# Kernel tuning notes

Hardware: AMD Instinct MI355X
Metric: run time of the kernel (lower is better)

## Reference

```python
import jax, jax.numpy as jnp
import numpy as np

P = 8  # patch size (hardcoded in unfold/fold of the original module)


def conv2d(x, w, b, groups=1):
    # x: (N,C,H,W), w: (O, C//groups, 3, 3), 'SAME' padding = padding=1 for 3x3
    y = jax.lax.conv_general_dilated(
        x, w, window_strides=(1, 1), padding='SAME',
        dimension_numbers=('NCHW', 'OIHW', 'NCHW'),
        feature_group_count=groups)
    return y + b[None, :, None, None]


def unfold8(x):
    # F.unfold(kernel=8, stride=8): (N,C,H,W) -> (N, C*64, L), channel-major then
    # kernel-row/col ordering, patches in row-major order.
    N, C, H, W = x.shape
    x = x.reshape(N, C, H // P, P, W // P, P)
    x = x.transpose(0, 1, 3, 5, 2, 4)        # N,C,ki,kj,nh,nw
    return x.reshape(N, C * P * P, (H // P) * (W // P))


def fold8(x, H, W):
    # inverse of unfold8 (non-overlapping, stride == kernel)
    N = x.shape[0]
    C = x.shape[1] // (P * P)
    x = x.reshape(N, C, P, P, H // P, W // P)
    x = x.transpose(0, 1, 4, 2, 5, 3)        # N,C,nh,ki,nw,kj
    return x.reshape(N, C, H, W)


def setup_inputs() -> dict:
    key = jax.random.key(0)
    ks = jax.random.split(key, 9)
    c = 64
    x = jax.random.normal(ks[0], (16, 7, c, 64, 64), dtype=jnp.float32)
    wq = jax.random.normal(ks[1], (c, 1, 3, 3), dtype=jnp.float32) * 0.05
    wk = jax.random.normal(ks[2], (c, 1, 3, 3), dtype=jnp.float32) * 0.05
    wv = jax.random.normal(ks[3], (c, c, 3, 3), dtype=jnp.float32) * 0.05
    wc = jax.random.normal(ks[4], (c, c, 3, 3), dtype=jnp.float32) * 0.05
    bq = jnp.zeros((c,), jnp.float32)
    bk = jnp.zeros((c,), jnp.float32)
    bv = jnp.zeros((c,), jnp.float32)
    bc = jnp.zeros((c,), jnp.float32)
    return {"x": x, "wq": wq, "bq": bq, "wk": wk, "bk": bk,
            "wv": wv, "bv": bv, "wc": wc, "bc": bc}


def reference(x, wq, bq, wk, bk, wv, bv, wc, bc):
    heads = 1
    b, t, c, h, w = x.shape
    D = P * P * c          # dim
    d = D // heads         # hidden_dim per head
    L = (h // P) * (w // P)  # num patches per frame

    xf = x.reshape(-1, c, h, w)
    q = unfold8(conv2d(xf, wq, bq, groups=c))   # depthwise conv
    k = unfold8(conv2d(xf, wk, bk, groups=c))   # depthwise conv
    v = unfold8(conv2d(xf, wv, bv))             # dense conv

    def rearr(u):
        # (b*t, D, L) -> (b, heads, d, t*L)
        return u.reshape(b, t, heads, d, L).transpose(0, 2, 3, 1, 4).reshape(b, heads, d, t * L)

    q, k, v = rearr(q), rearr(k), rearr(v)

    attn = jnp.einsum('bhds,bhdu->bhsu', q, k) * (d ** -0.5)  # (b,H,tL,tL)
    attn = jax.nn.softmax(attn, axis=-1)
    out = jnp.einsum('bhsu,bhdu->bhsd', attn, v)               # (b,H,tL,d)

    out = out.reshape(b, heads, t, L, d).transpose(0, 2, 1, 4, 3).reshape(b * t, D, L)
    feat = fold8(out, h, w)
    return conv2d(feat, wc, bc).reshape(x.shape) + x
```

## Files before the change

kernel.cpp:

```cpp
#include <hip/hip_runtime.h>
#include <hip/hip_bf16.h>


namespace {
constexpr int NFR = 112;
constexpr int T_  = 7;
constexpr int B_  = 16;
constexpr int C_  = 64;
constexpr int H_  = 64;
constexpr int W_  = 64;
constexpr int S_  = 448;
constexpr int D_  = 4096;
constexpr size_t QKV_E = (size_t)B_ * S_ * D_;
constexpr size_t ATTN_E = (size_t)B_ * S_ * S_;
}

typedef __attribute__((ext_vector_type(8))) short short8v;
typedef __attribute__((ext_vector_type(4))) float float4v;

__device__ __forceinline__ float bfu2f(unsigned short u) {
    union { unsigned int i; float f; } v; v.i = ((unsigned int)u) << 16; return v.f;
}
__device__ __forceinline__ unsigned short f2bf(float f) {
    __hip_bfloat16 h = __float2bfloat16(f);
    return *reinterpret_cast<unsigned short*>(&h);
}

__device__ __forceinline__ short8v frag_ld(const char* ldsb, int r, int kByte) {
    return *(const short8v*)(ldsb + r * 128 + (kByte ^ ((r & 7) << 4)));
}

template<int NTHR>
__device__ __forceinline__ void stage_tile(char* ldsb, const unsigned short* g,
                                           int ldg, int t) {
    #pragma unroll
    for (int i = 0; i < 1024 / NTHR; ++i) {
        int e = i * NTHR + t;
        int r = e >> 3, c8 = (e & 7) * 8;
        short8v v = *(const short8v*)(g + (size_t)r * ldg + c8);
        *(short8v*)(ldsb + r * 128 + ((c8 * 2) ^ ((r & 7) << 4))) = v;
    }
}

__device__ __forceinline__ void stage_vt(char* ldsb, const unsigned short* g, int t) {
    int d0 = (t & 15) * 8;
    int u0 = (t >> 4) * 4;
    short8v r0 = *(const short8v*)(g + (size_t)(u0 + 0) * D_ + d0);
    short8v r1 = *(const short8v*)(g + (size_t)(u0 + 1) * D_ + d0);
    short8v r2 = *(const short8v*)(g + (size_t)(u0 + 2) * D_ + d0);
    short8v r3 = *(const short8v*)(g + (size_t)(u0 + 3) * D_ + d0);
    #pragma unroll
    for (int j = 0; j < 8; ++j) {
        unsigned int lo = (unsigned short)r0[j] | (((unsigned int)(unsigned short)r1[j]) << 16);
        unsigned int hi = (unsigned short)r2[j] | (((unsigned int)(unsigned short)r3[j]) << 16);
        int d = d0 + j;
        int byte = d * 128 + (((unsigned)(u0 * 2)) ^ ((d & 7) << 4));
        *(uint2*)(ldsb + byte) = uint2{lo, hi};
    }
}

__global__ __launch_bounds__(256) void prep_w2(const float* __restrict__ wv,
                                               const float* __restrict__ wc,
                                               __hip_bfloat16* __restrict__ Wt_v,
                                               __hip_bfloat16* __restrict__ Wt_c)
{
    int t = blockIdx.x * 256 + threadIdx.x;
    if (t >= 2 * 36864) return;
    int which = t >= 36864;
    int i = t - which * 36864;
    const float* s = which ? wc : wv;
    __hip_bfloat16* d = which ? Wt_c : Wt_v;
    int r = i >> 12, co = (i >> 6) & 63, ci = i & 63;
    d[i] = __float2bfloat16(s[(co * 64 + ci) * 9 + r]);
}

template<bool IS_V>
__global__ __launch_bounds__(512, 4) void conv_mfma6(
    const void* __restrict__ src,
    const __hip_bfloat16* __restrict__ Wt,
    const float* __restrict__ bias,
    const float* __restrict__ xin,
    void* __restrict__ dst,
    const float* __restrict__ wq, const float* __restrict__ bq,
    const float* __restrict__ wk, const float* __restrict__ bk,
    unsigned short* __restrict__ Qout, unsigned short* __restrict__ Kout)
{
    __shared__ char xs[6 * 66 * 128];
    __shared__ char wl[2][64 * 128];
    __shared__ float wqk_s[IS_V ? 1280 : 1];
    const int f    = blockIdx.y;
    const int band = blockIdx.x;
    const int y0   = band * 4;
    const int tid  = threadIdx.x;
    const int lane = tid & 63;
    const int w    = tid >> 6;
    const int q    = lane >> 4;
    const int l15  = lane & 15;
    const int wrow = w >> 1;
    const int wco  = w & 1;

    const unsigned short* Wg = (const unsigned short*)Wt;
    const int r0w = tid >> 3, c0w = (tid & 7) * 8;
    const int wlo = r0w * 128 + ((c0w * 2) ^ ((r0w & 7) << 4));
    const unsigned short* wgl = Wg + r0w * 64 + c0w;

    short8v w0A = *(const short8v*)(wgl);

    if constexpr (IS_V) {
        for (int e = tid; e < 1280; e += 512) {
            float v;
            if (e < 576)       v = wq[e];
            else if (e < 1152) v = wk[e - 576];
            else if (e < 1216) v = bq[e - 1152];
            else               v = bk[e - 1216];
            wqk_s[e] = v;
        }
    }

    for (int e = tid; e < 6 * 16 * 64; e += 512) {
        int x  = e & 63;
        int cg = (e >> 6) & 15;
        int r  = e >> 10;
        int y  = y0 - 1 + r;
        unsigned short p[4];
        if ((unsigned)y < (unsigned)H_) {
            #pragma unroll
            for (int j = 0; j < 4; ++j) {
                size_t gi = (((size_t)f * C_ + cg * 4 + j) * H_ + y) * W_ + x;
                if constexpr (IS_V) p[j] = f2bf(((const float*)src)[gi]);
                else                p[j] = ((const unsigned short*)src)[gi];
            }
        } else { p[0] = p[1] = p[2] = p[3] = 0; }
        int xp = x + 1;
        int byte = (r * 66 + xp) * 128 + ((cg * 8) ^ ((xp & 7) << 4));
        *(uint2*)(xs + byte) = *(uint2*)p;
    }
    for (int e = tid; e < 6 * 16 * 2; e += 512) {
        int side = e & 1;
        int cg   = (e >> 1) & 15;
        int r    = e >> 5;
        int xp   = side ? 65 : 0;
        int byte = (r * 66 + xp) * 128 + ((cg * 8) ^ ((xp & 7) << 4));
        *(uint2*)(xs + byte) = uint2{0u, 0u};
    }
    *(short8v*)(wl[0] + wlo) = w0A;
    __syncthreads();

    float4v acc[4][2] = {};
    #pragma unroll
    for (int tap = 0; tap < 9; ++tap) {
        const int ky = tap / 3, kx = tap - ky * 3;
        short8v nwA;
        if (tap + 1 < 9) {
            nwA = *(const short8v*)(wgl + (tap + 1) * 4096);
            __builtin_amdgcn_sched_barrier(0);
        }
        const char* wb = wl[tap & 1];
        const int ri = wrow + ky;
        #pragma unroll
        for (int kc = 0; kc < 2; ++kc) {
            int kB = kc * 64 + q * 16;
            short8v bfr[2];
            #pragma unroll
            for (int nt = 0; nt < 2; ++nt)
                bfr[nt] = frag_ld(wb, wco * 32 + nt * 16 + l15, kB);
            #pragma unroll
            for (int xt = 0; xt < 4; ++xt) {
                int xp = xt * 16 + l15 + kx;
                short8v av = *(const short8v*)(xs + (ri * 66 + xp) * 128 +
                                               (kB ^ ((xp & 7) << 4)));
                #pragma unroll
                for (int nt = 0; nt < 2; ++nt)
                    acc[xt][nt] = __builtin_amdgcn_mfma_f32_16x16x32_bf16(
                        av, bfr[nt], acc[xt][nt], 0, 0, 0);
            }
        }
        if (tap + 1 < 9) {
            *(short8v*)(wl[(tap + 1) & 1] + wlo) = nwA;
        }
        __syncthreads();
    }

    float bco[2];
    #pragma unroll
    for (int nt = 0; nt < 2; ++nt) bco[nt] = bias[wco * 32 + nt * 16 + l15];
    const int bb = f / T_, tt = f % T_;
    const int R = y0 + wrow;
    #pragma unroll
    for (int xt = 0; xt < 4; ++xt) {
        #pragma unroll
        for (int nt = 0; nt < 2; ++nt) {
            int co = wco * 32 + nt * 16 + l15;
            if constexpr (IS_V) {
                int s  = tt * 64 + (R >> 3) * 8 + xt * 2 + (q >> 1);
                int d0 = co * 64 + (R & 7) * 8 + (q & 1) * 4;
                unsigned short pk[4];
                #pragma unroll
                for (int j = 0; j < 4; ++j)
                    pk[j] = f2bf(acc[xt][nt][j] + bco[nt]);
                *(uint2*)((unsigned short*)dst + ((size_t)bb * S_ + s) * D_ + d0) =
                    *(const uint2*)pk;
            } else {
                size_t o = (((size_t)f * C_ + co) * H_ + R) * W_ + xt * 16 + q * 4;
                float4 rv = *(const float4*)(xin + o);
                float4 ov;
                ov.x = acc[xt][nt][0] + bco[nt] + rv.x;
                ov.y = acc[xt][nt][1] + bco[nt] + rv.y;
                ov.z = acc[xt][nt][2] + bco[nt] + rv.z;
                ov.w = acc[xt][nt][3] + bco[nt] + rv.w;
                *(float4*)((float*)dst + o) = ov;
            }
        }
    }

    if constexpr (IS_V) {
        const int cg8  = lane >> 3;
        const int half = (lane >> 2) & 1;
        const int r2   = lane & 3;
        const int px   = w;
        const int yk   = ((band & 1) << 2) + r2;
        const int s    = tt * 64 + (band >> 1) * 8 + px;
        #pragma unroll
        for (int p = 0; p < 2; ++p) {
            const int c0 = cg8 * 8 + half * 4 + p * 2;
            float acq[2][8], ack[2][8];
            float bq0 = wqk_s[1152 + c0], bq1 = wqk_s[1152 + c0 + 1];
            float bk0 = wqk_s[1216 + c0], bk1 = wqk_s[1216 + c0 + 1];
            #pragma unroll
            for (int j = 0; j < 8; ++j) {
                acq[0][j] = bq0; acq[1][j] = bq1;
                ack[0][j] = bk0; ack[1][j] = bk1;
            }
            #pragma unroll
            for (int dy = 0; dy < 3; ++dy) {
                const int ri = r2 + dy;
                float rv0[10], rv1[10];
                #pragma unroll
                for (int u = 0; u < 10; ++u) {
                    int xp = px * 8 + u;
                    int byte = (ri * 66 + xp) * 128 + ((c0 * 2) ^ ((xp & 7) << 4));
                    unsigned int pr = *(const unsigned int*)(xs + byte);
                    rv0[u] = bfu2f((unsigned short)(pr & 0xffffu));
                    rv1[u] = bfu2f((unsigned short)(pr >> 16));
                }
                #pragma unroll
                for (int kx = 0; kx < 3; ++kx) {
                    float wq0 = wqk_s[c0 * 9 + dy * 3 + kx];
                    float wq1 = wqk_s[(c0 + 1) * 9 + dy * 3 + kx];
                    float wk0 = wqk_s[576 + c0 * 9 + dy * 3 + kx];
                    float wk1 = wqk_s[576 + (c0 + 1) * 9 + dy * 3 + kx];
                    #pragma unroll
                    for (int j = 0; j < 8; ++j) {
                        acq[0][j] += wq0 * rv0[j + kx];
                        acq[1][j] += wq1 * rv1[j + kx];
                        ack[0][j] += wk0 * rv0[j + kx];
                        ack[1][j] += wk1 * rv1[j + kx];
                    }
                }
            }
            #pragma unroll
            for (int i = 0; i < 2; ++i) {
                unsigned short pq[8], pk[8];
                #pragma unroll
                for (int j = 0; j < 8; ++j) {
                    pq[j] = f2bf(acq[i][j]);
                    pk[j] = f2bf(ack[i][j]);
                }
                size_t off = ((size_t)bb * S_ + s) * D_ + (size_t)(c0 + i) * 64 + yk * 8;
                *(short8v*)(Qout + off) = *(const short8v*)pq;
                *(short8v*)(Kout + off) = *(const short8v*)pk;
            }
        }
    }
}

__global__ __launch_bounds__(512, 2) void gemm_qk_mfma(
    const __hip_bfloat16* __restrict__ Qg,
    const __hip_bfloat16* __restrict__ Kg,
    float* __restrict__ ATTN)
{
    __shared__ alignas(16) char lds[32768];
    char* ldsA = lds;
    char* ldsB = lds + 16384;
    int bid = blockIdx.x;
    int lb  = (bid & 7) * 32 + (bid >> 3);
    int bb  = lb >> 4;
    int m0  = ((lb >> 2) & 3) * 128;
    int n0  = (lb & 3) * 128;
    const unsigned short* Ag = (const unsigned short*)Qg + (size_t)bb * S_ * D_ + (size_t)m0 * D_;
    const unsigned short* Bg = (const unsigned short*)Kg + (size_t)bb * S_ * D_ + (size_t)n0 * D_;
    int t = threadIdx.x;
    int w = t >> 6, l = t & 63, q = l >> 4, l15 = l & 15;
    int wm = w >> 2, wn = w & 3;
    int r0 = t >> 3, c0 = (t & 7) * 8;
    int r1 = 64 + r0;
    short8v sA0, sA1, sB0, sB1;
    sA0 = *(const short8v*)(Ag + (size_t)r0 * D_ + c0);
    sA1 = *(const short8v*)(Ag + (size_t)r1 * D_ + c0);
    sB0 = *(const short8v*)(Bg + (size_t)r0 * D_ + c0);
    sB1 = *(const short8v*)(Bg + (size_t)r1 * D_ + c0);

    float4v acc[4][2] = {};
    int swz0 = (c0 * 2) ^ ((r0 & 7) << 4);
    for (int k0 = 0; k0 < D_; k0 += 64) {
        __syncthreads();
        *(short8v*)(ldsA + r0 * 128 + swz0) = sA0;
        *(short8v*)(ldsA + r1 * 128 + swz0) = sA1;
        *(short8v*)(ldsB + r0 * 128 + swz0) = sB0;
        *(short8v*)(ldsB + r1 * 128 + swz0) = sB1;
        if (k0 + 64 < D_) {
            int kn = k0 + 64;
            sA0 = *(const short8v*)(Ag + (size_t)r0 * D_ + kn + c0);
            sA1 = *(const short8v*)(Ag + (size_t)r1 * D_ + kn + c0);
            sB0 = *(const short8v*)(Bg + (size_t)r0 * D_ + kn + c0);
            sB1 = *(const short8v*)(Bg + (size_t)r1 * D_ + kn + c0);
        }
        __syncthreads();
        #pragma unroll
        for (int kc = 0; kc < 2; ++kc) {
            int kB = kc * 64 + q * 16;
            short8v a[4], b[2];
            #pragma unroll
            for (int mt = 0; mt < 4; ++mt) a[mt] = frag_ld(ldsA, wm * 64 + mt * 16 + l15, kB);
            #pragma unroll
            for (int nt = 0; nt < 2; ++nt) b[nt] = frag_ld(ldsB, wn * 32 + nt * 16 + l15, kB);
            #pragma unroll
            for (int mt = 0; mt < 4; ++mt)
                #pragma unroll
                for (int nt = 0; nt < 2; ++nt)
                    acc[mt][nt] = __builtin_amdgcn_mfma_f32_16x16x32_bf16(
                        a[mt], b[nt], acc[mt][nt], 0, 0, 0);
        }
    }
    const float scale = 1.0f / 64.0f;
    #pragma unroll
    for (int mt = 0; mt < 4; ++mt) {
        #pragma unroll
        for (int nt = 0; nt < 2; ++nt) {
            int u = n0 + wn * 32 + nt * 16 + l15;
            #pragma unroll
            for (int j = 0; j < 4; ++j) {
                int s = m0 + wm * 64 + mt * 16 + q * 4 + j;
                if (s < S_ && u < S_)
                    ATTN[((size_t)bb * S_ + s) * S_ + u] = acc[mt][nt][j] * scale;
            }
        }
    }
}

__global__ __launch_bounds__(64) void softmax_rows(const float* __restrict__ ATTN,
                                                   unsigned short* __restrict__ P)
{
    size_t row = blockIdx.x;
    const float* p = ATTN + row * S_;
    int lane = threadIdx.x;
    float vals[7];
    float m = -1e30f;
    #pragma unroll
    for (int i = 0; i < 7; ++i) { vals[i] = p[lane + i * 64]; m = fmaxf(m, vals[i]); }
    #pragma unroll
    for (int off = 32; off; off >>= 1) m = fmaxf(m, __shfl_xor(m, off));
    float sum = 0.f;
    #pragma unroll
    for (int i = 0; i < 7; ++i) { vals[i] = __expf(vals[i] - m); sum += vals[i]; }
    #pragma unroll
    for (int off = 32; off; off >>= 1) sum += __shfl_xor(sum, off);
    float inv = 1.f / sum;
    #pragma unroll
    for (int i = 0; i < 7; ++i) P[row * S_ + lane + i * 64] = f2bf(vals[i] * inv);
}

__global__ __launch_bounds__(256, 2) void gemm_pv_mfma(
    const unsigned short* __restrict__ Pg,
    const __hip_bfloat16* __restrict__ Vg,
    __hip_bfloat16* __restrict__ FEAT)
{
    __shared__ alignas(16) char lds[32768];
    char* ldsA = lds;
    char* ldsB = lds + 16384;
    int bid = blockIdx.x;
    int lb  = (bid & 7) * 256 + (bid >> 3);
    int bb  = lb >> 7;
    int tl  = lb & 127;
    int m0  = (tl >> 5) * 128;
    int n0  = (tl & 31) * 128;
    const unsigned short* Ag = Pg + (size_t)bb * S_ * S_ + (size_t)m0 * S_;
    const unsigned short* Bg = (const unsigned short*)Vg + (size_t)bb * S_ * D_ + n0;
    int t = threadIdx.x;
    int w = t >> 6, l = t & 63, q = l >> 4, l15 = l & 15;
    int wm = w >> 1, wn = w & 1;
    float4v acc[4][4] = {};
    for (int k0 = 0; k0 < S_; k0 += 64) {
        __syncthreads();
        stage_tile<256>(ldsA, Ag + k0, S_, t);
        stage_vt(ldsB, Bg + (size_t)k0 * D_, t);
        __syncthreads();
        #pragma unroll
        for (int kc = 0; kc < 2; ++kc) {
            int kB = kc * 64 + q * 16;
            short8v a[4], b[4];
            #pragma unroll
            for (int mt = 0; mt < 4; ++mt) a[mt] = frag_ld(ldsA, wm * 64 + mt * 16 + l15, kB);
            #pragma unroll
            for (int nt = 0; nt < 4; ++nt) b[nt] = frag_ld(ldsB, wn * 64 + nt * 16 + l15, kB);
            #pragma unroll
            for (int mt = 0; mt < 4; ++mt)
                #pragma unroll
                for (int nt = 0; nt < 4; ++nt)
                    acc[mt][nt] = __builtin_amdgcn_mfma_f32_16x16x32_bf16(
                        a[mt], b[nt], acc[mt][nt], 0, 0, 0);
        }
    }
    #pragma unroll
    for (int mt = 0; mt < 4; ++mt) {
        #pragma unroll
        for (int j = 0; j < 4; ++j) {
            int s = m0 + wm * 64 + mt * 16 + q * 4 + j;
            if (s >= S_) continue;
            int f  = bb * T_ + (s >> 6);
            int l6 = s & 63;
            #pragma unroll
            for (int nt = 0; nt < 4; ++nt) {
                int d = n0 + wn * 64 + nt * 16 + l15;
                int c = d >> 6, r = d & 63;
                int y  = ((l6 >> 3) << 3) + (r >> 3);
                int xx = ((l6 & 7) << 3) + (r & 7);
                FEAT[(((size_t)f * C_ + c) * H_ + y) * W_ + xx] =
                    __float2bfloat16(acc[mt][nt][j]);
            }
        }
    }
}

extern "C" void kernel_launch(void* const* d_in, const int* in_sizes, int n_in,
                              void* d_out, int out_size, void* d_ws, size_t ws_size,
                              hipStream_t stream)
{
    const float* x  = (const float*)d_in[0];
    const float* wq = (const float*)d_in[1];
    const float* bq = (const float*)d_in[2];
    const float* wk = (const float*)d_in[3];
    const float* bk = (const float*)d_in[4];
    const float* wv = (const float*)d_in[5];
    const float* bv = (const float*)d_in[6];
    const float* wc = (const float*)d_in[7];
    const float* bc = (const float*)d_in[8];
    float* out = (float*)d_out;

    __hip_bfloat16* Qb = (__hip_bfloat16*)d_ws;
    __hip_bfloat16* Kb = Qb + QKV_E;
    __hip_bfloat16* Vb = Kb + QKV_E;
    float* ATTN = (float*)(Vb + QKV_E);
    __hip_bfloat16* Wt_v = (__hip_bfloat16*)(ATTN + ATTN_E);
    __hip_bfloat16* Wt_c = Wt_v + 9 * 64 * 64;
    unsigned short* Pb   = (unsigned short*)Kb;
    __hip_bfloat16* FEAT = Qb;

    prep_w2<<<288, 256, 0, stream>>>(wv, wc, Wt_v, Wt_c);

    conv_mfma6<true><<<dim3(16, NFR), 512, 0, stream>>>(
        x, Wt_v, bv, nullptr, Vb,
        wq, bq, wk, bk, (unsigned short*)Qb, (unsigned short*)Kb);
    gemm_qk_mfma<<<256, 512, 0, stream>>>(Qb, Kb, ATTN);
    softmax_rows<<<B_ * S_, 64, 0, stream>>>(ATTN, Pb);
    gemm_pv_mfma<<<2048, 256, 0, stream>>>(Pb, Vb, FEAT);
    conv_mfma6<false><<<dim3(16, NFR), 512, 0, stream>>>(
        FEAT, Wt_c, bc, x, out,
        nullptr, nullptr, nullptr, nullptr, nullptr, nullptr);
}
```

Measured before the change: 337.2 us.

## Split QK GEMM K-dimension across two half-blocks and remap Q/K conv lanes

The QK GEMM kernel now launches 1024 threads per block, and each 512-thread half reduces over its own half of the 4096-long K dimension. The two partial accumulators are then combined through LDS before scaling and storing. This doubles the waves working on each output tile of the 256-block grid, which should improve latency hiding, at the cost of more LDS and an extra reduction step. Separately, the depthwise Q/K lane mapping in the conv kernel is changed so each lane handles a channel pair across two rows, which alters the LDS read and global store access patterns.

```diff
diff --git a/kernel.cpp b/kernel.cpp
--- a/kernel.cpp
+++ b/kernel.cpp
@@ -214,15 +214,15 @@
     }
 
     if constexpr (IS_V) {
-        const int cg8  = lane >> 3;
-        const int half = (lane >> 2) & 1;
-        const int r2   = lane & 3;
+        const int c2   = lane & 31;
+        const int r2hi = lane >> 5;
+        const int c0   = c2 * 2;
         const int px   = w;
-        const int yk   = ((band & 1) << 2) + r2;
         const int s    = tt * 64 + (band >> 1) * 8 + px;
         #pragma unroll
-        for (int p = 0; p < 2; ++p) {
-            const int c0 = cg8 * 8 + half * 4 + p * 2;
+        for (int pi = 0; pi < 2; ++pi) {
+            const int r2 = r2hi * 2 + pi;
+            const int yk = ((band & 1) << 2) + r2;
             float acq[2][8], ack[2][8];
             float bq0 = wqk_s[1152 + c0], bq1 = wqk_s[1152 + c0 + 1];
             float bk0 = wqk_s[1216 + c0], bk1 = wqk_s[1216 + c0 + 1];
@@ -274,22 +274,26 @@
     }
 }
 
-__global__ __launch_bounds__(512, 2) void gemm_qk_mfma(
+__global__ __launch_bounds__(1024, 4) void gemm_qk_mfma(
     const __hip_bfloat16* __restrict__ Qg,
     const __hip_bfloat16* __restrict__ Kg,
     float* __restrict__ ATTN)
 {
-    __shared__ alignas(16) char lds[32768];
-    char* ldsA = lds;
-    char* ldsB = lds + 16384;
+    __shared__ alignas(16) char lds[65536];
+    const int tid = threadIdx.x;
+    const int kh  = tid >> 9;
+    const int t   = tid & 511;
+    char* ldsA = lds + kh * 32768;
+    char* ldsB = ldsA + 16384;
     int bid = blockIdx.x;
     int lb  = (bid & 7) * 32 + (bid >> 3);
     int bb  = lb >> 4;
     int m0  = ((lb >> 2) & 3) * 128;
     int n0  = (lb & 3) * 128;
-    const unsigned short* Ag = (const unsigned short*)Qg + (size_t)bb * S_ * D_ + (size_t)m0 * D_;
-    const unsigned short* Bg = (const unsigned short*)Kg + (size_t)bb * S_ * D_ + (size_t)n0 * D_;
-    int t = threadIdx.x;
+    const unsigned short* Ag = (const unsigned short*)Qg + (size_t)bb * S_ * D_
+                               + (size_t)m0 * D_ + kh * 2048;
+    const unsigned short* Bg = (const unsigned short*)Kg + (size_t)bb * S_ * D_
+                               + (size_t)n0 * D_ + kh * 2048;
     int w = t >> 6, l = t & 63, q = l >> 4, l15 = l & 15;
     int wm = w >> 2, wn = w & 3;
     int r0 = t >> 3, c0 = (t & 7) * 8;
@@ -302,13 +306,13 @@
 
     float4v acc[4][2] = {};
     int swz0 = (c0 * 2) ^ ((r0 & 7) << 4);
-    for (int k0 = 0; k0 < D_; k0 += 64) {
+    for (int k0 = 0; k0 < 2048; k0 += 64) {
         __syncthreads();
         *(short8v*)(ldsA + r0 * 128 + swz0) = sA0;
         *(short8v*)(ldsA + r1 * 128 + swz0) = sA1;
         *(short8v*)(ldsB + r0 * 128 + swz0) = sB0;
         *(short8v*)(ldsB + r1 * 128 + swz0) = sB1;
-        if (k0 + 64 < D_) {
+        if (k0 + 64 < 2048) {
             int kn = k0 + 64;
             sA0 = *(const short8v*)(Ag + (size_t)r0 * D_ + kn + c0);
             sA1 = *(const short8v*)(Ag + (size_t)r1 * D_ + kn + c0);
@@ -332,17 +336,31 @@
                         a[mt], b[nt], acc[mt][nt], 0, 0, 0);
         }
     }
-    const float scale = 1.0f / 64.0f;
-    #pragma unroll
-    for (int mt = 0; mt < 4; ++mt) {
-        #pragma unroll
-        for (int nt = 0; nt < 2; ++nt) {
-            int u = n0 + wn * 32 + nt * 16 + l15;
-            #pragma unroll
-            for (int j = 0; j < 4; ++j) {
-                int s = m0 + wm * 64 + mt * 16 + q * 4 + j;
-                if (s < S_ && u < S_)
-                    ATTN[((size_t)bb * S_ + s) * S_ + u] = acc[mt][nt][j] * scale;
+
+    __syncthreads();
+    if (kh) {
+        #pragma unroll
+        for (int mt = 0; mt < 4; ++mt)
+            #pragma unroll
+            for (int nt = 0; nt < 2; ++nt)
+                *(float4v*)(lds + (mt * 2 + nt) * 8192 + t * 16) = acc[mt][nt];
+    }
+    __syncthreads();
+    if (!kh) {
+        const float scale = 1.0f / 64.0f;
+        #pragma unroll
+        for (int mt = 0; mt < 4; ++mt) {
+            #pragma unroll
+            for (int nt = 0; nt < 2; ++nt) {
+                float4v o = *(const float4v*)(lds + (mt * 2 + nt) * 8192 + t * 16);
+                float4v v = acc[mt][nt];
+                int u = n0 + wn * 32 + nt * 16 + l15;
+                #pragma unroll
+                for (int j = 0; j < 4; ++j) {
+                    int s = m0 + wm * 64 + mt * 16 + q * 4 + j;
+                    if (s < S_ && u < S_)
+                        ATTN[((size_t)bb * S_ + s) * S_ + u] = (v[j] + o[j]) * scale;
+                }
             }
         }
     }
@@ -461,7 +479,7 @@
     conv_mfma6<true><<<dim3(16, NFR), 512, 0, stream>>>(
         x, Wt_v, bv, nullptr, Vb,
         wq, bq, wk, bk, (unsigned short*)Qb, (unsigned short*)Kb);
-    gemm_qk_mfma<<<256, 512, 0, stream>>>(Qb, Kb, ATTN);
+    gemm_qk_mfma<<<256, 1024, 0, stream>>>(Qb, Kb, ATTN);
     softmax_rows<<<B_ * S_, 64, 0, stream>>>(ATTN, Pb);
     gemm_pv_mfma<<<2048, 256, 0, stream>>>(Pb, Vb, FEAT);
     conv_mfma6<false><<<dim3(16, NFR), 512, 0, stream>>>(
```

Result: slower. 366.5 us (+8.7%).
